# Optimization experiments

Measured on AMD Instinct MI355X. Metric: run time of the kernel, lower is better.

Reference implementation:

```python
import jax, jax.numpy as jnp
import numpy as np

KSIZE = 3


def _windows(img, ksize):
    # img: [B, 1, H, W] -> [B, 1, H, W, ksize*ksize] sliding windows with reflect pad
    p = ksize // 2
    padded = jnp.pad(img, ((0, 0), (0, 0), (p, p), (p, p)), mode='reflect')
    H, W = img.shape[2], img.shape[3]
    wins = [padded[:, :, i:i + H, j:j + W] for i in range(ksize) for j in range(ksize)]
    return jnp.stack(wins, axis=-1)


def setup_inputs() -> dict:
    key = jax.random.key(0)
    x = jax.random.normal(key, (8, 3, 512, 512), dtype=jnp.float32)
    return {"x": x}


def reference(x):
    ksize = KSIZE
    center_idx = x.shape[1] // 2
    center = x[:, center_idx:center_idx + 1]            # [B,1,H,W]
    wins = _windows(center, ksize)                      # [B,1,H,W,k*k]
    med = jnp.median(wins, axis=-1)                     # local median (odd k*k -> exact element)
    mad = jnp.median(jnp.abs(wins - med[..., None]), axis=-1)  # median abs deviation
    return mad
```

## Files before the change

kernel.cpp:

```cpp
#include <hip/hip_runtime.h>
#include <hip/hip_bf16.h>

__device__ __forceinline__ void ce(float& a, float& b) {
    float t = fminf(a, b); b = fmaxf(a, b); a = t;
}
__device__ __forceinline__ void s3(float& a, float& b, float& c) {
    ce(a, b); ce(a, c); ce(b, c);
}

__device__ __forceinline__ void merge21(float x0, float x1, float y0,
                                        float& p0, float& p1, float& p2) {
    ce(x0, y0);
    p0 = x0; p1 = y0; p2 = x1; ce(p1, p2);
}

__device__ __forceinline__ void merge33(float a0, float a1, float a2,
                                        float b0, float b1, float b2,
                                        float& w0, float& w1, float& w2,
                                        float& w3, float& w4, float& w5) {
    float x0 = a0, x1 = a2, y0 = b0, y1 = b2;
    ce(x0, y0); ce(x1, y1); ce(x1, y0);
    float e0 = a1, e1 = b1; ce(e0, e1);
    w0 = x0;
    w1 = x1; w2 = e0; ce(w1, w2);
    w3 = y0; w4 = e1; ce(w3, w4);
    w5 = y1;
}

__device__ __forceinline__ void merge63(float c0, float c1, float c2, float c3, float c4, float c5,
                                        float d0, float d1, float d2,
                                        float& w0, float& w1, float& w2, float& w3, float& w4,
                                        float& w5, float& w6, float& w7, float& w8) {
    float p0, p1, p2; merge21(c0, c4, d0, p0, p1, p2);
    float q0 = c2, q1 = d2; ce(q0, q1);
    float o0 = p0, o1 = p1, o2 = q0; ce(o1, o2);
    float o3 = p2, o4 = q1; ce(o3, o4);
    float r0, r1, r2; merge21(c1, c5, d1, r0, r1, r2);
    float e0 = r0, e1 = r1, e2 = c3; ce(e1, e2);
    float e3 = r2;
    w0 = o0;
    w1 = o1; w2 = e0; ce(w1, w2);
    w3 = o2; w4 = e1; ce(w3, w4);
    w5 = o3; w6 = e2; ce(w5, w6);
    w7 = o4; w8 = e3; ce(w7, w8);
}

__device__ __forceinline__ float mad_sorted9(float w0, float w1, float w2, float w3, float w4,
                                             float w5, float w6, float w7, float w8) {
    float m = w4;
    float m0 = fminf(m - w3, w8 - m);
    float m1 = fminf(m - w2, w7 - m);
    float m2 = fminf(m - w1, w6 - m);
    float m3 = fminf(m - w0, w5 - m);
    return fmaxf(fmaxf(m0, m1), fmaxf(m2, m3));
}

__device__ __forceinline__ float mad_px(float c0, float c1, float c2, float c3, float c4, float c5,
                                        float d0, float d1, float d2) {
    float w0, w1, w2, w3, w4, w5, w6, w7, w8;
    merge63(c0, c1, c2, c3, c4, c5, d0, d1, d2, w0, w1, w2, w3, w4, w5, w6, w7, w8);
    return mad_sorted9(w0, w1, w2, w3, w4, w5, w6, w7, w8);
}

__global__ void __launch_bounds__(256)
mad_kernel(const float* __restrict__ x, float* __restrict__ out) {
    const int W = 512;
    int idx = blockIdx.x * blockDim.x + threadIdx.x;
    int g  = idx & 127;
    int py = (idx >> 7) & 511;
    int b  = idx >> 16;
    int px0 = g << 2;

    const float* base = x + ((size_t)(b * 3 + 1)) * (512 * 512);

    int ym = (py == 0)   ? 1   : py - 1;
    int yp = (py == 511) ? 510 : py + 1;

    const float* r0 = base + ym * W;
    const float* r1 = base + py * W;
    const float* r2 = base + yp * W;

    int xl = (px0 == 0)   ? 1   : px0 - 1;
    int xr = (px0 == 508) ? 510 : px0 + 4;

    float4 c0 = *reinterpret_cast<const float4*>(r0 + px0);
    float4 c1 = *reinterpret_cast<const float4*>(r1 + px0);
    float4 c2 = *reinterpret_cast<const float4*>(r2 + px0);
    float l0 = r0[xl], l1 = r1[xl], l2 = r2[xl];
    float q0 = r0[xr], q1 = r1[xr], q2 = r2[xr];

    float A0 = l0,   A1 = l1,   A2 = l2;   s3(A0, A1, A2);
    float B0 = c0.x, B1 = c1.x, B2 = c2.x; s3(B0, B1, B2);
    float C0 = c0.y, C1 = c1.y, C2 = c2.y; s3(C0, C1, C2);
    float D0 = c0.z, D1 = c1.z, D2 = c2.z; s3(D0, D1, D2);
    float E0 = c0.w, E1 = c1.w, E2 = c2.w; s3(E0, E1, E2);
    float F0 = q0,   F1 = q1,   F2 = q2;   s3(F0, F1, F2);

    float M01_0, M01_1, M01_2, M01_3, M01_4, M01_5;
    merge33(A0, A1, A2, B0, B1, B2, M01_0, M01_1, M01_2, M01_3, M01_4, M01_5);
    float M23_0, M23_1, M23_2, M23_3, M23_4, M23_5;
    merge33(C0, C1, C2, D0, D1, D2, M23_0, M23_1, M23_2, M23_3, M23_4, M23_5);
    float M45_0, M45_1, M45_2, M45_3, M45_4, M45_5;
    merge33(E0, E1, E2, F0, F1, F2, M45_0, M45_1, M45_2, M45_3, M45_4, M45_5);

    float4 o;
    o.x = mad_px(M01_0, M01_1, M01_2, M01_3, M01_4, M01_5, C0, C1, C2);
    o.y = mad_px(M23_0, M23_1, M23_2, M23_3, M23_4, M23_5, B0, B1, B2);
    o.z = mad_px(M23_0, M23_1, M23_2, M23_3, M23_4, M23_5, E0, E1, E2);
    o.w = mad_px(M45_0, M45_1, M45_2, M45_3, M45_4, M45_5, D0, D1, D2);

    *reinterpret_cast<float4*>(out + ((size_t)idx << 2)) = o;
}

extern "C" void kernel_launch(void* const* d_in, const int* in_sizes, int n_in,
                              void* d_out, int out_size, void* d_ws, size_t ws_size,
                              hipStream_t stream) {
    const float* x = (const float*)d_in[0];
    float* out = (float*)d_out;
    const int groups = 8 * 512 * 128;
    const int block = 256;
    const int grid = groups / block;
    mad_kernel<<<grid, block, 0, stream>>>(x, out);
}
```

Measured before the change: 11.42 us.

## Process 8 pixels per thread with wavefront shuffles for row halos

Each wavefront now covers one full image row, and each thread computes 8 output pixels instead of 4. Left and right halo columns come from neighbour lanes via shuffles rather than extra scalar global loads. Sorted column triples and pairwise merges are shared across more outputs, which cuts per-pixel sorting work and redundant loads. The trade-offs are half as many threads, higher register pressure, and reliance on a 64-wide wavefront for the shuffle layout.

```diff
diff --git a/kernel.cpp b/kernel.cpp
--- a/kernel.cpp
+++ b/kernel.cpp
@@ -55,23 +55,22 @@
     return fmaxf(fmaxf(m0, m1), fmaxf(m2, m3));
 }
 
-__device__ __forceinline__ float mad_px(float c0, float c1, float c2, float c3, float c4, float c5,
-                                        float d0, float d1, float d2) {
+__device__ __forceinline__ float mad_px(const float* pm, const float* d) {
     float w0, w1, w2, w3, w4, w5, w6, w7, w8;
-    merge63(c0, c1, c2, c3, c4, c5, d0, d1, d2, w0, w1, w2, w3, w4, w5, w6, w7, w8);
+    merge63(pm[0], pm[1], pm[2], pm[3], pm[4], pm[5], d[0], d[1], d[2],
+            w0, w1, w2, w3, w4, w5, w6, w7, w8);
     return mad_sorted9(w0, w1, w2, w3, w4, w5, w6, w7, w8);
 }
 
 __global__ void __launch_bounds__(256)
 mad_kernel(const float* __restrict__ x, float* __restrict__ out) {
     const int W = 512;
-    int idx = blockIdx.x * blockDim.x + threadIdx.x;
-    int g  = idx & 127;
-    int py = (idx >> 7) & 511;
-    int b  = idx >> 16;
-    int px0 = g << 2;
+    int lane = threadIdx.x & 63;
+    int wid  = threadIdx.x >> 6;
+    int rowg = blockIdx.x * 4 + wid;
+    int py = rowg & 511;
 
-    const float* base = x + ((size_t)(b * 3 + 1)) * (512 * 512);
+    const float* base = x + ((size_t)((rowg >> 9) * 3 + 1)) * (512 * 512);
 
     int ym = (py == 0)   ? 1   : py - 1;
     int yp = (py == 511) ? 510 : py + 1;
@@ -80,36 +79,51 @@
     const float* r1 = base + py * W;
     const float* r2 = base + yp * W;
 
-    int xl = (px0 == 0)   ? 1   : px0 - 1;
-    int xr = (px0 == 508) ? 510 : px0 + 4;
+    int c = lane << 3;
+    float4 a0 = *reinterpret_cast<const float4*>(r0 + c);
+    float4 b0 = *reinterpret_cast<const float4*>(r0 + c + 4);
+    float4 a1 = *reinterpret_cast<const float4*>(r1 + c);
+    float4 b1 = *reinterpret_cast<const float4*>(r1 + c + 4);
+    float4 a2 = *reinterpret_cast<const float4*>(r2 + c);
+    float4 b2 = *reinterpret_cast<const float4*>(r2 + c + 4);
 
-    float4 c0 = *reinterpret_cast<const float4*>(r0 + px0);
-    float4 c1 = *reinterpret_cast<const float4*>(r1 + px0);
-    float4 c2 = *reinterpret_cast<const float4*>(r2 + px0);
-    float l0 = r0[xl], l1 = r1[xl], l2 = r2[xl];
-    float q0 = r0[xr], q1 = r1[xr], q2 = r2[xr];
+    float L0 = __shfl_up(b0.w, 1), L1 = __shfl_up(b1.w, 1), L2 = __shfl_up(b2.w, 1);
+    float R0 = __shfl_down(a0.x, 1), R1 = __shfl_down(a1.x, 1), R2 = __shfl_down(a2.x, 1);
+    if (lane == 0)  { L0 = a0.y; L1 = a1.y; L2 = a2.y; }
+    if (lane == 63) { R0 = b0.z; R1 = b1.z; R2 = b2.z; }
 
-    float A0 = l0,   A1 = l1,   A2 = l2;   s3(A0, A1, A2);
-    float B0 = c0.x, B1 = c1.x, B2 = c2.x; s3(B0, B1, B2);
-    float C0 = c0.y, C1 = c1.y, C2 = c2.y; s3(C0, C1, C2);
-    float D0 = c0.z, D1 = c1.z, D2 = c2.z; s3(D0, D1, D2);
-    float E0 = c0.w, E1 = c1.w, E2 = c2.w; s3(E0, E1, E2);
-    float F0 = q0,   F1 = q1,   F2 = q2;   s3(F0, F1, F2);
+    float col[10][3];
+    col[0][0] = L0;   col[0][1] = L1;   col[0][2] = L2;
+    col[1][0] = a0.x; col[1][1] = a1.x; col[1][2] = a2.x;
+    col[2][0] = a0.y; col[2][1] = a1.y; col[2][2] = a2.y;
+    col[3][0] = a0.z; col[3][1] = a1.z; col[3][2] = a2.z;
+    col[4][0] = a0.w; col[4][1] = a1.w; col[4][2] = a2.w;
+    col[5][0] = b0.x; col[5][1] = b1.x; col[5][2] = b2.x;
+    col[6][0] = b0.y; col[6][1] = b1.y; col[6][2] = b2.y;
+    col[7][0] = b0.z; col[7][1] = b1.z; col[7][2] = b2.z;
+    col[8][0] = b0.w; col[8][1] = b1.w; col[8][2] = b2.w;
+    col[9][0] = R0;   col[9][1] = R1;   col[9][2] = R2;
+#pragma unroll
+    for (int i = 0; i < 10; ++i) s3(col[i][0], col[i][1], col[i][2]);
 
-    float M01_0, M01_1, M01_2, M01_3, M01_4, M01_5;
-    merge33(A0, A1, A2, B0, B1, B2, M01_0, M01_1, M01_2, M01_3, M01_4, M01_5);
-    float M23_0, M23_1, M23_2, M23_3, M23_4, M23_5;
-    merge33(C0, C1, C2, D0, D1, D2, M23_0, M23_1, M23_2, M23_3, M23_4, M23_5);
-    float M45_0, M45_1, M45_2, M45_3, M45_4, M45_5;
-    merge33(E0, E1, E2, F0, F1, F2, M45_0, M45_1, M45_2, M45_3, M45_4, M45_5);
+    float pm[5][6];
+#pragma unroll
+    for (int i = 0; i < 5; ++i)
+        merge33(col[2*i][0], col[2*i][1], col[2*i][2],
+                col[2*i+1][0], col[2*i+1][1], col[2*i+1][2],
+                pm[i][0], pm[i][1], pm[i][2], pm[i][3], pm[i][4], pm[i][5]);
 
-    float4 o;
-    o.x = mad_px(M01_0, M01_1, M01_2, M01_3, M01_4, M01_5, C0, C1, C2);
-    o.y = mad_px(M23_0, M23_1, M23_2, M23_3, M23_4, M23_5, B0, B1, B2);
-    o.z = mad_px(M23_0, M23_1, M23_2, M23_3, M23_4, M23_5, E0, E1, E2);
-    o.w = mad_px(M45_0, M45_1, M45_2, M45_3, M45_4, M45_5, D0, D1, D2);
+    float o[8];
+#pragma unroll
+    for (int j = 0; j < 8; ++j) {
+        const int pi = (j + 1) >> 1;
+        const int ei = (j & 1) ? j : j + 2;
+        o[j] = mad_px(pm[pi], col[ei]);
+    }
 
-    *reinterpret_cast<float4*>(out + ((size_t)idx << 2)) = o;
+    float* orow = out + (size_t)rowg * W + c;
+    *reinterpret_cast<float4*>(orow)     = make_float4(o[0], o[1], o[2], o[3]);
+    *reinterpret_cast<float4*>(orow + 4) = make_float4(o[4], o[5], o[6], o[7]);
 }
 
 extern "C" void kernel_launch(void* const* d_in, const int* in_sizes, int n_in,
@@ -117,8 +131,8 @@
                               hipStream_t stream) {
     const float* x = (const float*)d_in[0];
     float* out = (float*)d_out;
-    const int groups = 8 * 512 * 128;
+    const int rows = 8 * 512;
     const int block = 256;
-    const int grid = groups / block;
+    const int grid = rows / 4;
     mad_kernel<<<grid, block, 0, stream>>>(x, out);
 }
```

Result: faster. 10.64 us (-6.9%).
